# Performance work log

Hardware: AMD Instinct MI355X
Metric: run time of the kernel (lower is better)

The kernel has to match this reference:

```python
import jax, jax.numpy as jnp
import numpy as np

N_NODES = 100000
N_EDGES = 1200000
D_IN = 64
D_HID = 64
D_OUT = 64


def setup_inputs() -> dict:
    key = jax.random.key(0)
    k1, k2, k3, k4, k5, k6 = jax.random.split(key, 6)
    x = jax.random.normal(k1, (N_NODES, D_IN), dtype=jnp.float32)
    edge_index = jax.random.randint(k2, (2, N_EDGES), 0, N_NODES, dtype=jnp.int32)
    s1 = 1.0 / np.sqrt(2 * D_IN)
    s2 = 1.0 / np.sqrt(2 * D_HID)
    W1 = jax.random.uniform(k3, (2 * D_IN, D_HID), jnp.float32, -s1, s1)
    b1 = jax.random.uniform(k4, (D_HID,), jnp.float32, -s1, s1)
    W2 = jax.random.uniform(k5, (2 * D_HID, D_OUT), jnp.float32, -s2, s2)
    b2 = jax.random.uniform(k6, (D_OUT,), jnp.float32, -s2, s2)
    return {"x": x, "edge_index": edge_index, "W1": W1, "b1": b1, "W2": W2, "b2": b2}


def _sage_conv(x, row, col, W, b):
    n = x.shape[0]
    # gather neighbor features and scatter-sum to destinations
    neighbor_sum = jax.ops.segment_sum(x[col], row, num_segments=n)  # [N, d]
    deg = jax.ops.segment_sum(jnp.ones(row.shape[0], x.dtype), row, num_segments=n)
    deg = jnp.maximum(deg, 1.0)
    neighbor_agg = neighbor_sum / deg[:, None]
    out = jnp.concatenate([x, neighbor_agg], axis=-1)  # [N, 2d]
    return out @ W + b


def reference(x, edge_index, W1, b1, W2, b2):
    row, col = edge_index[0], edge_index[1]
    h = jax.nn.relu(_sage_conv(x, row, col, W1, b1))
    # dropout is identity at inference (training=False)
    return _sage_conv(h, row, col, W2, b2)
```

## Files before the change

### kernel.cpp

```cpp
#include <hip/hip_runtime.h>

#define N_NODES 100000
#define N_EDGES 1200000
#define D 64

#define BSHIFT 10
#define NB ((N_NODES + 1023) >> BSHIFT)
#define EPB 2048
#define P1_BLOCKS ((N_EDGES + EPB - 1) / EPB)
#define P2_CAP 16384

typedef short bf16x8 __attribute__((ext_vector_type(8)));
typedef float f32x4 __attribute__((ext_vector_type(4)));
typedef unsigned short u16x4 __attribute__((ext_vector_type(4)));
typedef unsigned short u16x8 __attribute__((ext_vector_type(8)));

__device__ __forceinline__ short f2bf(float x) {
  unsigned u = __float_as_uint(x);
  unsigned r = (u + 0x7FFFu + ((u >> 16) & 1u)) >> 16;
  return (short)r;
}
__device__ __forceinline__ float bf2f(short b) {
  return __uint_as_float(((unsigned)(unsigned short)b) << 16);
}

__global__ __launch_bounds__(256) void cvt_bf(const float* __restrict__ in,
                                              unsigned short* __restrict__ o,
                                              int n8) {
  int i = blockIdx.x * 256 + threadIdx.x;
  if (i >= n8) return;
  const float4 a0 = *(const float4*)(in + (size_t)i * 8);
  const float4 a1 = *(const float4*)(in + (size_t)i * 8 + 4);
  const float f[8] = {a0.x, a0.y, a0.z, a0.w, a1.x, a1.y, a1.z, a1.w};
  u16x8 v;
#pragma unroll
  for (int j = 0; j < 8; ++j) v[j] = (unsigned short)f2bf(f[j]);
  *(u16x8*)(o + (size_t)i * 8) = v;
}

__global__ __launch_bounds__(256) void p1_count(const int* __restrict__ row,
                                                int* __restrict__ bucketCount) {
  __shared__ int h[NB];
  const int t = threadIdx.x;
  for (int i = t; i < NB; i += 256) h[i] = 0;
  __syncthreads();
  const int base = blockIdx.x * EPB;
#pragma unroll
  for (int i = 0; i < EPB / 256; ++i) {
    int e = base + i * 256 + t;
    if (e < N_EDGES) atomicAdd(&h[row[e] >> BSHIFT], 1);
  }
  __syncthreads();
  for (int i = t; i < NB; i += 256)
    if (h[i]) atomicAdd(&bucketCount[i], h[i]);
}

__global__ __launch_bounds__(128) void p1_scan(const int* __restrict__ bucketCount,
                                               int* __restrict__ bucketStart,
                                               int* __restrict__ cursor) {
  __shared__ int lds[128];
  const int t = threadIdx.x;
  int v = (t < NB) ? bucketCount[t] : 0;
  lds[t] = v;
  __syncthreads();
  for (int off = 1; off < 128; off <<= 1) {
    int add = (t >= off) ? lds[t - off] : 0;
    __syncthreads();
    lds[t] += add;
    __syncthreads();
  }
  if (t < NB) {
    int start = lds[t] - v;
    bucketStart[t] = start;
    cursor[t] = start;
  }
  if (t == NB - 1) bucketStart[NB] = lds[t];
}

__global__ __launch_bounds__(256) void p1_scatter(
    const int* __restrict__ row, const int* __restrict__ col,
    int* __restrict__ cursor, unsigned long long* __restrict__ pairBuf) {
  __shared__ int h[NB];
  __shared__ int hexcl[NB];
  __shared__ int gbase[NB];
  __shared__ int scan_lds[128];
  __shared__ unsigned long long staged[EPB];
  const int t = threadIdx.x;
  for (int i = t; i < NB; i += 256) h[i] = 0;
  __syncthreads();
  const int base = blockIdx.x * EPB;
  const int cnt = min(EPB, N_EDGES - base);

  int myrank[EPB / 256];
  int mybkt[EPB / 256];
  unsigned long long mypair[EPB / 256];
#pragma unroll
  for (int i = 0; i < EPB / 256; ++i) {
    int e = base + i * 256 + t;
    if (e < N_EDGES) {
      unsigned r = (unsigned)row[e];
      unsigned c = (unsigned)col[e];
      int b = (int)(r >> BSHIFT);
      mybkt[i] = b;
      mypair[i] = ((unsigned long long)r << 32) | c;
      myrank[i] = atomicAdd(&h[b], 1);
    } else {
      mybkt[i] = -1;
    }
  }
  __syncthreads();
  int v = 0;
  if (t < 128) { v = (t < NB) ? h[t] : 0; scan_lds[t] = v; }
  __syncthreads();
  for (int off = 1; off < 128; off <<= 1) {
    int add = (t >= off && t < 128) ? scan_lds[t - off] : 0;
    __syncthreads();
    if (t < 128) scan_lds[t] += add;
    __syncthreads();
  }
  if (t < NB) {
    hexcl[t] = scan_lds[t] - v;
    gbase[t] = (h[t] > 0) ? atomicAdd(&cursor[t], h[t]) : 0;
  }
  __syncthreads();
#pragma unroll
  for (int i = 0; i < EPB / 256; ++i)
    if (mybkt[i] >= 0) staged[hexcl[mybkt[i]] + myrank[i]] = mypair[i];
  __syncthreads();
  for (int i = t; i < cnt; i += 256) {
    unsigned long long p = staged[i];
    int b = (int)(p >> (32 + BSHIFT));
    pairBuf[gbase[b] + (i - hexcl[b])] = p;
  }
}

__global__ __launch_bounds__(1024) void p2_csr(
    const unsigned long long* __restrict__ pairBuf,
    const int* __restrict__ bucketStart,
    int* __restrict__ ends, int* __restrict__ sortedCol) {
  __shared__ int hist[1024];
  __shared__ int sc[1024];
  __shared__ unsigned short rankLDS[P2_CAP];
  const int t = threadIdx.x;
  const int b = blockIdx.x;
  const int base = bucketStart[b];
  const int cnt = min(bucketStart[b + 1] - base, P2_CAP);
  hist[t] = 0;
  __syncthreads();
  for (int i = t; i < cnt; i += 1024) {
    int lr = (int)((pairBuf[base + i] >> 32) & ((1 << BSHIFT) - 1));
    rankLDS[i] = (unsigned short)atomicAdd(&hist[lr], 1);
  }
  __syncthreads();
  int v = hist[t];
  sc[t] = v;
  __syncthreads();
  for (int off = 1; off < 1024; off <<= 1) {
    int add = (t >= off) ? sc[t - off] : 0;
    __syncthreads();
    sc[t] += add;
    __syncthreads();
  }
  const int node = (b << BSHIFT) + t;
  if (node < N_NODES) ends[node] = base + sc[t];
  const int excl = sc[t] - v;
  __syncthreads();
  sc[t] = excl;
  __syncthreads();
  for (int i = t; i < cnt; i += 1024) {
    unsigned long long p = pairBuf[base + i];
    int lr = (int)((p >> 32) & ((1 << BSHIFT) - 1));
    sortedCol[base + sc[lr] + (int)rankLDS[i]] = (int)(unsigned)p;
  }
}

__global__ __launch_bounds__(256) void sage_agg(
    const unsigned short* __restrict__ xb, const int* __restrict__ ends,
    const int* __restrict__ sortedCol, unsigned short* __restrict__ agg, int n) {
  const int lane = threadIdx.x & 63;
  const int g = lane >> 4;
  const int fq = lane & 15;
  const int gwave = (blockIdx.x * blockDim.x + threadIdx.x) >> 6;
  const int nwaves = (gridDim.x * blockDim.x) >> 6;

  for (int r = gwave; r < n; r += nwaves) {
    const int start = (r == 0) ? 0 : ends[r - 1];
    const int end = ends[r];
    const int deg = end - start;
    float4 acc = make_float4(0.f, 0.f, 0.f, 0.f);

    for (int base = start; base < end; base += 64) {
      const int m = min(64, end - base);
      const int cv = (lane < m) ? sortedCol[base + lane] : 0;
      for (int j = 0; j < m; j += 16) {
        const int i0 = j + 0 + g, i1 = j + 4 + g, i2 = j + 8 + g, i3 = j + 12 + g;
        const int c0 = __shfl(cv, i0 < m ? i0 : 0);
        const int c1 = __shfl(cv, i1 < m ? i1 : 0);
        const int c2 = __shfl(cv, i2 < m ? i2 : 0);
        const int c3 = __shfl(cv, i3 < m ? i3 : 0);
        u16x4 v0, v1, v2, v3;
        if (i0 < m) v0 = *(const u16x4*)(xb + (size_t)c0 * D + fq * 4);
        if (i1 < m) v1 = *(const u16x4*)(xb + (size_t)c1 * D + fq * 4);
        if (i2 < m) v2 = *(const u16x4*)(xb + (size_t)c2 * D + fq * 4);
        if (i3 < m) v3 = *(const u16x4*)(xb + (size_t)c3 * D + fq * 4);
        if (i0 < m) { acc.x += bf2f(v0[0]); acc.y += bf2f(v0[1]);
                      acc.z += bf2f(v0[2]); acc.w += bf2f(v0[3]); }
        if (i1 < m) { acc.x += bf2f(v1[0]); acc.y += bf2f(v1[1]);
                      acc.z += bf2f(v1[2]); acc.w += bf2f(v1[3]); }
        if (i2 < m) { acc.x += bf2f(v2[0]); acc.y += bf2f(v2[1]);
                      acc.z += bf2f(v2[2]); acc.w += bf2f(v2[3]); }
        if (i3 < m) { acc.x += bf2f(v3[0]); acc.y += bf2f(v3[1]);
                      acc.z += bf2f(v3[2]); acc.w += bf2f(v3[3]); }
      }
    }
    acc.x += __shfl_xor(acc.x, 16); acc.x += __shfl_xor(acc.x, 32);
    acc.y += __shfl_xor(acc.y, 16); acc.y += __shfl_xor(acc.y, 32);
    acc.z += __shfl_xor(acc.z, 16); acc.z += __shfl_xor(acc.z, 32);
    acc.w += __shfl_xor(acc.w, 16); acc.w += __shfl_xor(acc.w, 32);
    if (g == 0) {
      const float s = 1.0f / (float)max(deg, 1);
      u16x4 o;
      o[0] = (unsigned short)f2bf(acc.x * s);
      o[1] = (unsigned short)f2bf(acc.y * s);
      o[2] = (unsigned short)f2bf(acc.z * s);
      o[3] = (unsigned short)f2bf(acc.w * s);
      *(u16x4*)(agg + (size_t)r * D + fq * 4) = o;
    }
  }
}

__global__ __launch_bounds__(256) void w_swizzle(const float* __restrict__ W,
                                                 short* __restrict__ wh,
                                                 short* __restrict__ wl) {
  int i = blockIdx.x * blockDim.x + threadIdx.x;
  if (i >= 4 * 4 * 64 * 8) return;
  int j = i & 7;
  int l = (i >> 3) & 63;
  int s = (i >> 9) & 3;
  int t = i >> 11;
  int k = s * 32 + ((l >> 4) * 8) + j;
  int n = t * 16 + (l & 15);
  float v = W[k * 64 + n];
  short hb = f2bf(v);
  short lb = f2bf(v - bf2f(hb));
  wh[i] = hb;
  wl[i] = lb;
}

__global__ __launch_bounds__(256) void sage_mm(
    const float* __restrict__ xin, const unsigned short* __restrict__ aggb,
    const short* __restrict__ wh, const short* __restrict__ wl,
    const float* __restrict__ b, float* __restrict__ out,
    unsigned short* __restrict__ hb, int doRelu) {
  const int lane = threadIdx.x & 63;
  const int m = lane & 15;
  const int q = lane >> 4;
  const int gwave = (blockIdx.x * blockDim.x + threadIdx.x) >> 6;
  const int nwaves = (gridDim.x * blockDim.x) >> 6;
  const int nTiles = N_NODES / 16;

  for (int tile = gwave; tile < nTiles; tile += nwaves) {
    const int r0 = tile * 16;
    f32x4 acc[4];
#pragma unroll
    for (int t = 0; t < 4; ++t) {
      const float bv = b[t * 16 + m];
      acc[t][0] = bv; acc[t][1] = bv; acc[t][2] = bv; acc[t][3] = bv;
    }

#pragma unroll
    for (int s = 0; s < 4; ++s) {
      const int kb = (s & 1) * 32 + q * 8;
      bf16x8 Ah, Al;
      if (s < 2) {
        const float* rowp = xin + (size_t)(r0 + m) * D + kb;
        const float4 a0 = *(const float4*)rowp;
        const float4 a1 = *(const float4*)(rowp + 4);
        const float f[8] = {a0.x, a0.y, a0.z, a0.w, a1.x, a1.y, a1.z, a1.w};
#pragma unroll
        for (int j = 0; j < 8; ++j) {
          const short hv = f2bf(f[j]);
          Ah[j] = hv;
          Al[j] = f2bf(f[j] - bf2f(hv));
        }
      } else {
        Ah = *(const bf16x8*)(aggb + (size_t)(r0 + m) * D + kb);
      }
#pragma unroll
      for (int t = 0; t < 4; ++t) {
        const int bi = ((t * 4 + s) * 64 + lane) * 8;
        const bf16x8 Bh = *(const bf16x8*)(wh + bi);
        const bf16x8 Bl = *(const bf16x8*)(wl + bi);
        acc[t] = __builtin_amdgcn_mfma_f32_16x16x32_bf16(Ah, Bh, acc[t], 0, 0, 0);
        acc[t] = __builtin_amdgcn_mfma_f32_16x16x32_bf16(Ah, Bl, acc[t], 0, 0, 0);
        if (s < 2)
          acc[t] = __builtin_amdgcn_mfma_f32_16x16x32_bf16(Al, Bh, acc[t], 0, 0, 0);
      }
    }

#pragma unroll
    for (int t = 0; t < 4; ++t) {
#pragma unroll
      for (int rg = 0; rg < 4; ++rg) {
        float v = acc[t][rg];
        if (doRelu) v = fmaxf(v, 0.0f);
        const size_t oi = (size_t)(r0 + q * 4 + rg) * D + t * 16 + m;
        out[oi] = v;
        if (doRelu) hb[oi] = (unsigned short)f2bf(v);
      }
    }
  }
}

extern "C" void kernel_launch(void* const* d_in, const int* in_sizes, int n_in,
                              void* d_out, int out_size, void* d_ws, size_t ws_size,
                              hipStream_t stream) {
  const float* x  = (const float*)d_in[0];
  const int*   ei = (const int*)d_in[1];
  const float* W1 = (const float*)d_in[2];
  const float* b1 = (const float*)d_in[3];
  const float* W2 = (const float*)d_in[4];
  const float* b2 = (const float*)d_in[5];
  float* out = (float*)d_out;

  const int* row = ei;
  const int* col = ei + N_EDGES;

  char* ws = (char*)d_ws;
  int* endsArr = (int*)ws;
  size_t off = ((size_t)N_NODES * sizeof(int) + 4095) & ~(size_t)4095;
  int* sortedCol = (int*)(ws + off);
  off += ((size_t)N_EDGES * sizeof(int) + 4095) & ~(size_t)4095;
  int* bucketCount = (int*)(ws + off);
  int* bucketStart = bucketCount + 128;
  int* cursor = bucketStart + 256;
  off += 4096;
  short* w1h = (short*)(ws + off); off += 8192 * sizeof(short);
  short* w1l = (short*)(ws + off); off += 8192 * sizeof(short);
  short* w2h = (short*)(ws + off); off += 8192 * sizeof(short);
  short* w2l = (short*)(ws + off); off += 8192 * sizeof(short);
  unsigned short* xh = (unsigned short*)(ws + off);
  off += (size_t)N_NODES * D * sizeof(unsigned short);
  unsigned short* hb = (unsigned short*)(ws + off);
  off += (size_t)N_NODES * D * sizeof(unsigned short);
  off = (off + 4095) & ~(size_t)4095;
  unsigned long long* pairBuf = (unsigned long long*)(ws + off);
  unsigned short* aggbf = (unsigned short*)(ws + off);

  hipMemsetAsync(bucketCount, 0, NB * sizeof(int), stream);

  w_swizzle<<<32, 256, 0, stream>>>(W1, w1h, w1l);
  w_swizzle<<<32, 256, 0, stream>>>(W2, w2h, w2l);
  cvt_bf<<<(N_NODES * D / 8 + 255) / 256, 256, 0, stream>>>(x, xh, N_NODES * D / 8);

  p1_count<<<P1_BLOCKS, 256, 0, stream>>>(row, bucketCount);
  p1_scan<<<1, 128, 0, stream>>>(bucketCount, bucketStart, cursor);
  p1_scatter<<<P1_BLOCKS, 256, 0, stream>>>(row, col, cursor, pairBuf);
  p2_csr<<<NB, 1024, 0, stream>>>(pairBuf, bucketStart, endsArr, sortedCol);

  sage_agg<<<2048, 256, 0, stream>>>(xh, endsArr, sortedCol, aggbf, N_NODES);
  sage_mm<<<1024, 256, 0, stream>>>(x, aggbf, w1h, w1l, b1, out, hb, 1);

  sage_agg<<<2048, 256, 0, stream>>>(hb, endsArr, sortedCol, aggbf, N_NODES);
  sage_mm<<<1024, 256, 0, stream>>>(out, aggbf, w2h, w2l, b2, out, hb, 0);
}
```

Baseline: 237.5 us.

## Precompute bf16 hi/lo splits, fuse prep kernels, and use finer CSR buckets

Fuses the weight swizzles and x conversion into one prep kernel that also emits a bf16 low-part array. The matmul then reads precomputed hi/lo bf16 operands instead of converting fp32 rows, and layer 1 writes only the hi/lo hidden arrays rather than fp32 out. CSR bucketing shrinks to 256 nodes per bucket with 256-thread p2 blocks and 512-thread scatter/scan. This cuts conversion work and fp32 traffic, but adds the extra low-part writes. The smaller per-bucket capacity of 4096 risks truncating overfull buckets.

Result: no change. 234.3 us (-1.3%).

```diff
diff --git a/kernel.cpp b/kernel.cpp
--- a/kernel.cpp
+++ b/kernel.cpp
@@ -4,11 +4,11 @@
 #define N_EDGES 1200000
 #define D 64
 
-#define BSHIFT 10
-#define NB ((N_NODES + 1023) >> BSHIFT)
+#define BSHIFT 8
+#define NB ((N_NODES + 255) >> BSHIFT)
 #define EPB 2048
 #define P1_BLOCKS ((N_EDGES + EPB - 1) / EPB)
-#define P2_CAP 16384
+#define P2_CAP 4096
 
 typedef short bf16x8 __attribute__((ext_vector_type(8)));
 typedef float f32x4 __attribute__((ext_vector_type(4)));
@@ -24,18 +24,44 @@
   return __uint_as_float(((unsigned)(unsigned short)b) << 16);
 }
 
-__global__ __launch_bounds__(256) void cvt_bf(const float* __restrict__ in,
-                                              unsigned short* __restrict__ o,
-                                              int n8) {
-  int i = blockIdx.x * 256 + threadIdx.x;
-  if (i >= n8) return;
-  const float4 a0 = *(const float4*)(in + (size_t)i * 8);
-  const float4 a1 = *(const float4*)(in + (size_t)i * 8 + 4);
+__device__ __forceinline__ void w_swz(const float* __restrict__ W,
+                                      short* __restrict__ wh,
+                                      short* __restrict__ wl, int blk) {
+  int i = blk * 256 + threadIdx.x;
+  int j = i & 7;
+  int l = (i >> 3) & 63;
+  int s = (i >> 9) & 3;
+  int t = i >> 11;
+  int k = s * 32 + ((l >> 4) * 8) + j;
+  int n = t * 16 + (l & 15);
+  float v = W[k * 64 + n];
+  short hb = f2bf(v);
+  wh[i] = hb;
+  wl[i] = f2bf(v - bf2f(hb));
+}
+
+__global__ __launch_bounds__(256) void prep(
+    const float* __restrict__ x, unsigned short* __restrict__ xh,
+    unsigned short* __restrict__ xl,
+    const float* __restrict__ W1, short* __restrict__ w1h, short* __restrict__ w1l,
+    const float* __restrict__ W2, short* __restrict__ w2h, short* __restrict__ w2l) {
+  const int bid = blockIdx.x;
+  if (bid < 32) { w_swz(W1, w1h, w1l, bid); return; }
+  if (bid < 64) { w_swz(W2, w2h, w2l, bid - 32); return; }
+  int i = (bid - 64) * 256 + threadIdx.x;
+  if (i >= N_NODES * D / 8) return;
+  const float4 a0 = *(const float4*)(x + (size_t)i * 8);
+  const float4 a1 = *(const float4*)(x + (size_t)i * 8 + 4);
   const float f[8] = {a0.x, a0.y, a0.z, a0.w, a1.x, a1.y, a1.z, a1.w};
-  u16x8 v;
-#pragma unroll
-  for (int j = 0; j < 8; ++j) v[j] = (unsigned short)f2bf(f[j]);
-  *(u16x8*)(o + (size_t)i * 8) = v;
+  u16x8 vh, vl;
+#pragma unroll
+  for (int j = 0; j < 8; ++j) {
+    const short hb = f2bf(f[j]);
+    vh[j] = (unsigned short)hb;
+    vl[j] = (unsigned short)f2bf(f[j] - bf2f(hb));
+  }
+  *(u16x8*)(xh + (size_t)i * 8) = vh;
+  *(u16x8*)(xl + (size_t)i * 8) = vl;
 }
 
 __global__ __launch_bounds__(256) void p1_count(const int* __restrict__ row,
@@ -55,15 +81,15 @@
     if (h[i]) atomicAdd(&bucketCount[i], h[i]);
 }
 
-__global__ __launch_bounds__(128) void p1_scan(const int* __restrict__ bucketCount,
+__global__ __launch_bounds__(512) void p1_scan(const int* __restrict__ bucketCount,
                                                int* __restrict__ bucketStart,
                                                int* __restrict__ cursor) {
-  __shared__ int lds[128];
+  __shared__ int lds[512];
   const int t = threadIdx.x;
   int v = (t < NB) ? bucketCount[t] : 0;
   lds[t] = v;
   __syncthreads();
-  for (int off = 1; off < 128; off <<= 1) {
+  for (int off = 1; off < 512; off <<= 1) {
     int add = (t >= off) ? lds[t - off] : 0;
     __syncthreads();
     lds[t] += add;
@@ -77,26 +103,26 @@
   if (t == NB - 1) bucketStart[NB] = lds[t];
 }
 
-__global__ __launch_bounds__(256) void p1_scatter(
+__global__ __launch_bounds__(512) void p1_scatter(
     const int* __restrict__ row, const int* __restrict__ col,
     int* __restrict__ cursor, unsigned long long* __restrict__ pairBuf) {
   __shared__ int h[NB];
   __shared__ int hexcl[NB];
   __shared__ int gbase[NB];
-  __shared__ int scan_lds[128];
+  __shared__ int scan_lds[512];
   __shared__ unsigned long long staged[EPB];
   const int t = threadIdx.x;
-  for (int i = t; i < NB; i += 256) h[i] = 0;
+  for (int i = t; i < NB; i += 512) h[i] = 0;
   __syncthreads();
   const int base = blockIdx.x * EPB;
   const int cnt = min(EPB, N_EDGES - base);
 
-  int myrank[EPB / 256];
-  int mybkt[EPB / 256];
-  unsigned long long mypair[EPB / 256];
-#pragma unroll
-  for (int i = 0; i < EPB / 256; ++i) {
-    int e = base + i * 256 + t;
+  int myrank[EPB / 512];
+  int mybkt[EPB / 512];
+  unsigned long long mypair[EPB / 512];
+#pragma unroll
+  for (int i = 0; i < EPB / 512; ++i) {
+    int e = base + i * 512 + t;
     if (e < N_EDGES) {
       unsigned r = (unsigned)row[e];
       unsigned c = (unsigned)col[e];
@@ -109,13 +135,13 @@
     }
   }
   __syncthreads();
-  int v = 0;
-  if (t < 128) { v = (t < NB) ? h[t] : 0; scan_lds[t] = v; }
-  __syncthreads();
-  for (int off = 1; off < 128; off <<= 1) {
-    int add = (t >= off && t < 128) ? scan_lds[t - off] : 0;
-    __syncthreads();
-    if (t < 128) scan_lds[t] += add;
+  int v = (t < NB) ? h[t] : 0;
+  scan_lds[t] = v;
+  __syncthreads();
+  for (int off = 1; off < 512; off <<= 1) {
+    int add = (t >= off) ? scan_lds[t - off] : 0;
+    __syncthreads();
+    scan_lds[t] += add;
     __syncthreads();
   }
   if (t < NB) {
@@ -124,22 +150,22 @@
   }
   __syncthreads();
 #pragma unroll
-  for (int i = 0; i < EPB / 256; ++i)
+  for (int i = 0; i < EPB / 512; ++i)
     if (mybkt[i] >= 0) staged[hexcl[mybkt[i]] + myrank[i]] = mypair[i];
   __syncthreads();
-  for (int i = t; i < cnt; i += 256) {
+  for (int i = t; i < cnt; i += 512) {
     unsigned long long p = staged[i];
     int b = (int)(p >> (32 + BSHIFT));
     pairBuf[gbase[b] + (i - hexcl[b])] = p;
   }
 }
 
-__global__ __launch_bounds__(1024) void p2_csr(
+__global__ __launch_bounds__(256) void p2_csr(
     const unsigned long long* __restrict__ pairBuf,
     const int* __restrict__ bucketStart,
     int* __restrict__ ends, int* __restrict__ sortedCol) {
-  __shared__ int hist[1024];
-  __shared__ int sc[1024];
+  __shared__ int hist[256];
+  __shared__ int sc[256];
   __shared__ unsigned short rankLDS[P2_CAP];
   const int t = threadIdx.x;
   const int b = blockIdx.x;
@@ -147,7 +173,7 @@
   const int cnt = min(bucketStart[b + 1] - base, P2_CAP);
   hist[t] = 0;
   __syncthreads();
-  for (int i = t; i < cnt; i += 1024) {
+  for (int i = t; i < cnt; i += 256) {
     int lr = (int)((pairBuf[base + i] >> 32) & ((1 << BSHIFT) - 1));
     rankLDS[i] = (unsigned short)atomicAdd(&hist[lr], 1);
   }
@@ -155,7 +181,7 @@
   int v = hist[t];
   sc[t] = v;
   __syncthreads();
-  for (int off = 1; off < 1024; off <<= 1) {
+  for (int off = 1; off < 256; off <<= 1) {
     int add = (t >= off) ? sc[t - off] : 0;
     __syncthreads();
     sc[t] += add;
@@ -167,7 +193,7 @@
   __syncthreads();
   sc[t] = excl;
   __syncthreads();
-  for (int i = t; i < cnt; i += 1024) {
+  for (int i = t; i < cnt; i += 256) {
     unsigned long long p = pairBuf[base + i];
     int lr = (int)((p >> 32) & ((1 << BSHIFT) - 1));
     sortedCol[base + sc[lr] + (int)rankLDS[i]] = (int)(unsigned)p;
@@ -229,29 +255,13 @@
   }
 }
 
-__global__ __launch_bounds__(256) void w_swizzle(const float* __restrict__ W,
-                                                 short* __restrict__ wh,
-                                                 short* __restrict__ wl) {
-  int i = blockIdx.x * blockDim.x + threadIdx.x;
-  if (i >= 4 * 4 * 64 * 8) return;
-  int j = i & 7;
-  int l = (i >> 3) & 63;
-  int s = (i >> 9) & 3;
-  int t = i >> 11;
-  int k = s * 32 + ((l >> 4) * 8) + j;
-  int n = t * 16 + (l & 15);
-  float v = W[k * 64 + n];
-  short hb = f2bf(v);
-  short lb = f2bf(v - bf2f(hb));
-  wh[i] = hb;
-  wl[i] = lb;
-}
-
 __global__ __launch_bounds__(256) void sage_mm(
-    const float* __restrict__ xin, const unsigned short* __restrict__ aggb,
+    const unsigned short* __restrict__ ah, const unsigned short* __restrict__ al,
+    const unsigned short* __restrict__ aggb,
     const short* __restrict__ wh, const short* __restrict__ wl,
     const float* __restrict__ b, float* __restrict__ out,
-    unsigned short* __restrict__ hb, int doRelu) {
+    unsigned short* __restrict__ hh, unsigned short* __restrict__ hl,
+    int doRelu) {
   const int lane = threadIdx.x & 63;
   const int m = lane & 15;
   const int q = lane >> 4;
@@ -271,20 +281,13 @@
 #pragma unroll
     for (int s = 0; s < 4; ++s) {
       const int kb = (s & 1) * 32 + q * 8;
+      const size_t ai = (size_t)(r0 + m) * D + kb;
       bf16x8 Ah, Al;
       if (s < 2) {
-        const float* rowp = xin + (size_t)(r0 + m) * D + kb;
-        const float4 a0 = *(const float4*)rowp;
-        const float4 a1 = *(const float4*)(rowp + 4);
-        const float f[8] = {a0.x, a0.y, a0.z, a0.w, a1.x, a1.y, a1.z, a1.w};
-#pragma unroll
-        for (int j = 0; j < 8; ++j) {
-          const short hv = f2bf(f[j]);
-          Ah[j] = hv;
-          Al[j] = f2bf(f[j] - bf2f(hv));
-        }
+        Ah = *(const bf16x8*)(ah + ai);
+        Al = *(const bf16x8*)(al + ai);
       } else {
-        Ah = *(const bf16x8*)(aggb + (size_t)(r0 + m) * D + kb);
+        Ah = *(const bf16x8*)(aggb + ai);
       }
 #pragma unroll
       for (int t = 0; t < 4; ++t) {
@@ -303,10 +306,15 @@
 #pragma unroll
       for (int rg = 0; rg < 4; ++rg) {
         float v = acc[t][rg];
-        if (doRelu) v = fmaxf(v, 0.0f);
         const size_t oi = (size_t)(r0 + q * 4 + rg) * D + t * 16 + m;
-        out[oi] = v;
-        if (doRelu) hb[oi] = (unsigned short)f2bf(v);
+        if (doRelu) {
+          v = fmaxf(v, 0.0f);
+          const short hv = f2bf(v);
+          hh[oi] = (unsigned short)hv;
+          hl[oi] = (unsigned short)f2bf(v - bf2f(hv));
+        } else {
+          out[oi] = v;
+        }
       }
     }
   }
@@ -332,16 +340,20 @@
   int* sortedCol = (int*)(ws + off);
   off += ((size_t)N_EDGES * sizeof(int) + 4095) & ~(size_t)4095;
   int* bucketCount = (int*)(ws + off);
-  int* bucketStart = bucketCount + 128;
-  int* cursor = bucketStart + 256;
-  off += 4096;
+  int* bucketStart = bucketCount + 512;
+  int* cursor = bucketStart + 512;
+  off += 8192;
   short* w1h = (short*)(ws + off); off += 8192 * sizeof(short);
   short* w1l = (short*)(ws + off); off += 8192 * sizeof(short);
   short* w2h = (short*)(ws + off); off += 8192 * sizeof(short);
   short* w2l = (short*)(ws + off); off += 8192 * sizeof(short);
   unsigned short* xh = (unsigned short*)(ws + off);
   off += (size_t)N_NODES * D * sizeof(unsigned short);
-  unsigned short* hb = (unsigned short*)(ws + off);
+  unsigned short* xl = (unsigned short*)(ws + off);
+  off += (size_t)N_NODES * D * sizeof(unsigned short);
+  unsigned short* hh = (unsigned short*)(ws + off);
+  off += (size_t)N_NODES * D * sizeof(unsigned short);
+  unsigned short* hl = (unsigned short*)(ws + off);
   off += (size_t)N_NODES * D * sizeof(unsigned short);
   off = (off + 4095) & ~(size_t)4095;
   unsigned long long* pairBuf = (unsigned long long*)(ws + off);
@@ -349,18 +361,17 @@
 
   hipMemsetAsync(bucketCount, 0, NB * sizeof(int), stream);
 
-  w_swizzle<<<32, 256, 0, stream>>>(W1, w1h, w1l);
-  w_swizzle<<<32, 256, 0, stream>>>(W2, w2h, w2l);
-  cvt_bf<<<(N_NODES * D / 8 + 255) / 256, 256, 0, stream>>>(x, xh, N_NODES * D / 8);
+  prep<<<64 + (N_NODES * D / 8 + 255) / 256, 256, 0, stream>>>(
+      x, xh, xl, W1, w1h, w1l, W2, w2h, w2l);
 
   p1_count<<<P1_BLOCKS, 256, 0, stream>>>(row, bucketCount);
-  p1_scan<<<1, 128, 0, stream>>>(bucketCount, bucketStart, cursor);
-  p1_scatter<<<P1_BLOCKS, 256, 0, stream>>>(row, col, cursor, pairBuf);
-  p2_csr<<<NB, 1024, 0, stream>>>(pairBuf, bucketStart, endsArr, sortedCol);
+  p1_scan<<<1, 512, 0, stream>>>(bucketCount, bucketStart, cursor);
+  p1_scatter<<<P1_BLOCKS, 512, 0, stream>>>(row, col, cursor, pairBuf);
+  p2_csr<<<NB, 256, 0, stream>>>(pairBuf, bucketStart, endsArr, sortedCol);
 
   sage_agg<<<2048, 256, 0, stream>>>(xh, endsArr, sortedCol, aggbf, N_NODES);
-  sage_mm<<<1024, 256, 0, stream>>>(x, aggbf, w1h, w1l, b1, out, hb, 1);
-
-  sage_agg<<<2048, 256, 0, stream>>>(hb, endsArr, sortedCol, aggbf, N_NODES);
-  sage_mm<<<1024, 256, 0, stream>>>(out, aggbf, w2h, w2l, b2, out, hb, 0);
-}
+  sage_mm<<<1563, 256, 0, stream>>>(xh, xl, aggbf, w1h, w1l, b1, out, hh, hl, 1);
+
+  sage_agg<<<2048, 256, 0, stream>>>(hh, endsArr, sortedCol, aggbf, N_NODES);
+  sage_mm<<<1563, 256, 0, stream>>>(hh, hl, aggbf, w2h, w2l, b2, out, hh, hl, 0);
+}
```
